# Optimization experiments

Measured on AMD Instinct MI355X. Metric: run time of the kernel, lower is better.

Reference implementation:

```python
import jax, jax.numpy as jnp
import numpy as np
import math

DIM = 384
HEADS = 6
HID = 32  # PositionalEncodingFourier hidden_dim
B, H, W = 16, 56, 56


def _layer_norm(x, g, b, eps=1e-6):
    mu = jnp.mean(x, axis=-1, keepdims=True)
    var = jnp.mean((x - mu) ** 2, axis=-1, keepdims=True)
    return (x - mu) * jax.lax.rsqrt(var + eps) * g + b


def _pos_encoding_fourier(Bb, Hh, Ww, w, b):
    # EdgeNeXt PositionalEncodingFourier with all-False mask: cumsum == arange+1
    scale = 2.0 * math.pi
    y_embed = jnp.arange(1, Hh + 1, dtype=jnp.float32)[:, None] / (Hh + 1e-6) * scale
    x_embed = jnp.arange(1, Ww + 1, dtype=jnp.float32)[None, :] / (Ww + 1e-6) * scale
    dim_t = 10000.0 ** (2.0 * (jnp.arange(HID) // 2).astype(jnp.float32) / HID)
    def enc(e):
        p = jnp.broadcast_to(e, (Hh, Ww))[..., None] / dim_t  # (H,W,HID)
        return jnp.stack([jnp.sin(p[..., 0::2]), jnp.cos(p[..., 1::2])], axis=-1).reshape(Hh, Ww, HID)
    pos = jnp.concatenate([enc(y_embed), enc(x_embed)], axis=-1)  # (H,W,2*HID)
    pos = pos @ w.T + b  # 1x1 conv token_projection as matmul -> (H,W,DIM)
    return jnp.broadcast_to(jnp.transpose(pos, (2, 0, 1))[None], (Bb, DIM, Hh, Ww))


def _forward(x, pos_w, pos_b, ln_g, ln_b, gamma_xca, temperature,
             qkv_w, qkv_b, proj_w, proj_b, rpb_table, conv_w,
             bn_g, bn_b, bn_mean, bn_var, gamma):
    Bb, C, Hh, Ww = x.shape
    N = Hh * Ww
    d = C // HEADS
    xt = jnp.transpose(x.reshape(Bb, C, N), (0, 2, 1))  # (B,N,C)
    pos = _pos_encoding_fourier(Bb, Hh, Ww, pos_w, pos_b)
    xt = xt + jnp.transpose(pos.reshape(Bb, C, N), (0, 2, 1))

    # relative position bias (seq_len T=2): gather (T,T,h) -> expand (h,d^2,T,T)
    # -> nearest interp x0.5 selects element (0,0) -> pixel_shuffle(d) of constant
    # channels == per-head scalar broadcast over the (d,d) channel-attention map.
    T = 2
    rel_idx = jnp.arange(T)[:, None] - jnp.arange(T)[None, :] + T - 1  # (2,2)
    rpb = rpb_table[rel_idx.reshape(-1)].reshape(T, T, HEADS)
    bias = rpb[0, 0][None, :, None, None]  # (1,heads,1,1), broadcasts over (d,d)

    # XCA: cross-covariance (channel) attention
    xn = _layer_norm(xt, ln_g, ln_b)
    qkv = (xn @ qkv_w.T + qkv_b).reshape(Bb, N, 3, HEADS, d)
    qkv = jnp.transpose(qkv, (2, 0, 3, 4, 1))  # (3,B,h,d,N)
    q, k, v = qkv[0], qkv[1], qkv[2]
    q = q / jnp.maximum(jnp.linalg.norm(q, axis=-1, keepdims=True), 1e-12)
    k = k / jnp.maximum(jnp.linalg.norm(k, axis=-1, keepdims=True), 1e-12)
    attn = jnp.einsum('bhdn,bhen->bhde', q, k) * temperature + bias  # (B,h,d,d)
    attn = jax.nn.softmax(attn, axis=-1)
    out = jnp.einsum('bhde,bhen->bhdn', attn, v)  # (B,h,d,N)
    out = jnp.transpose(out, (0, 3, 1, 2)).reshape(Bb, N, C)
    out = out @ proj_w.T + proj_b
    xt = xt + gamma_xca * out

    x2 = jnp.transpose(xt, (0, 2, 1)).reshape(Bb, C, Hh, Ww)
    # pwconv0: conv3x3 (dim->dim, expan_ration hardcoded to 1) + BN(inference) + SiLU
    xi = jax.lax.conv_general_dilated(x2, conv_w, (1, 1), [(1, 1), (1, 1)],
                                      dimension_numbers=('NCHW', 'OIHW', 'NCHW'))
    xi = (xi - bn_mean[None, :, None, None]) * jax.lax.rsqrt(bn_var + 1e-5)[None, :, None, None]
    xi = xi * bn_g[None, :, None, None] + bn_b[None, :, None, None]
    xi = xi * jax.nn.sigmoid(xi)  # SiLU
    x2 = x2 + xi

    # faithful to source: raw reshape (NOT permute) of contiguous NCHW into (B,H,W,C)
    x3 = x2.reshape(Bb, Hh, Ww, C) * gamma
    x3 = jnp.transpose(x3, (0, 3, 1, 2))
    return x + x3


def setup_inputs() -> dict:
    key = jax.random.key(0)
    ks = jax.random.split(key, 10)
    d3 = 3 * DIM
    return {
        'x': jax.random.normal(ks[0], (B, DIM, H, W), jnp.float32),
        'pos_w': jax.random.normal(ks[1], (DIM, 2 * HID), jnp.float32) * 0.05,
        'pos_b': jnp.zeros((DIM,), jnp.float32),
        'ln_g': jnp.ones((DIM,), jnp.float32),
        'ln_b': jnp.zeros((DIM,), jnp.float32),
        'gamma_xca': jax.random.normal(ks[2], (DIM,), jnp.float32) * 0.1,
        'temperature': jnp.ones((HEADS, 1, 1), jnp.float32),
        'qkv_w': jax.random.normal(ks[3], (d3, DIM), jnp.float32) * (DIM ** -0.5),
        'qkv_b': jnp.zeros((d3,), jnp.float32),
        'proj_w': jax.random.normal(ks[4], (DIM, DIM), jnp.float32) * (DIM ** -0.5),
        'proj_b': jnp.zeros((DIM,), jnp.float32),
        'rpb_table': jax.random.normal(ks[5], (3, HEADS), jnp.float32) * 0.02,
        'conv_w': jax.random.normal(ks[6], (DIM, DIM, 3, 3), jnp.float32) * 0.02,
        'bn_g': jnp.ones((DIM,), jnp.float32),
        'bn_b': jnp.zeros((DIM,), jnp.float32),
        'bn_mean': jax.random.normal(ks[7], (DIM,), jnp.float32) * 0.1,
        'bn_var': jax.random.uniform(ks[8], (DIM,), jnp.float32, 0.5, 1.5),
        'gamma': jax.random.normal(ks[9], (DIM,), jnp.float32) * 0.1,
    }


def reference(x, pos_w, pos_b, ln_g, ln_b, gamma_xca, temperature,
              qkv_w, qkv_b, proj_w, proj_b, rpb_table, conv_w,
              bn_g, bn_b, bn_mean, bn_var, gamma):
    return _forward(x, pos_w, pos_b, ln_g, ln_b, gamma_xca, temperature,
                    qkv_w, qkv_b, proj_w, proj_b, rpb_table, conv_w,
                    bn_g, bn_b, bn_mean, bn_var, gamma)
```

## Files before the change

### kernel.cpp

```cpp
#include <hip/hip_runtime.h>
#include <hip/hip_bf16.h>
#include <math.h>

#define DIM 384
#define HEADS 6
#define NN 3136
#define BB 16
#define BH (BB*HEADS)
#define HP 58
#define NP (HP*HP)

typedef __attribute__((ext_vector_type(8))) short short8;
typedef __attribute__((ext_vector_type(4))) short short4v;
typedef __attribute__((ext_vector_type(4))) float f32x4;

__device__ __forceinline__ float bf2f(unsigned short u) {
    union { unsigned int i; float f; } v; v.i = ((unsigned int)u) << 16; return v.f;
}
__device__ __forceinline__ unsigned short f2bf(float f) {
    union { float f; unsigned int i; } v; v.f = f;
    unsigned int r = v.i + 0x7fffu + ((v.i >> 16) & 1u);
    return (unsigned short)(r >> 16);
}
__device__ __forceinline__ void glds16(const unsigned short* g, void* l) {
    __builtin_amdgcn_global_load_lds(
        (const __attribute__((address_space(1))) unsigned int*)g,
        (__attribute__((address_space(3))) unsigned int*)l, 16, 0, 0);
}

__global__ void kw_convert(const float* __restrict__ qkv_w, const float* __restrict__ proj_w,
                           const float* __restrict__ conv_w,
                           unsigned short* __restrict__ Wq, unsigned short* __restrict__ Wp,
                           unsigned short* __restrict__ Wc) {
    int tid = blockIdx.x * 256 + threadIdx.x;
    int stride = gridDim.x * 256;
    for (int i = tid; i < 3*DIM*DIM; i += stride) Wq[i] = f2bf(qkv_w[i]);
    for (int i = tid; i < DIM*DIM; i += stride) Wp[i] = f2bf(proj_w[i]);
    for (int i = tid; i < DIM*DIM*9; i += stride) {
        int ii = i % DIM; int rest = i / DIM; int tap = rest % 9; int o = rest / 9;
        Wc[i] = f2bf(conv_w[(size_t)(o*DIM + ii)*9 + tap]);
    }
}

__global__ void k_pos(const float* __restrict__ pos_w, const float* __restrict__ pos_b,
                      float* __restrict__ P) {
    int n = blockIdx.x; int h = n / 56, w = n % 56;
    __shared__ float feat[64];
    int t = threadIdx.x;
    if (t < 64) {
        int axis = t >> 5;
        int k = t & 31; int i = k >> 1;
        float e = (float)((axis ? w : h) + 1) / 56.000001f * 6.28318530717958647692f;
        float arg = e / powf(10000.0f, (float)i / 16.0f);
        feat[t] = (k & 1) ? cosf(arg) : sinf(arg);
    }
    __syncthreads();
    for (int c = t; c < DIM; c += blockDim.x) {
        float s = pos_b[c];
        #pragma unroll 8
        for (int k = 0; k < 64; k++) s += feat[k] * pos_w[c*64 + k];
        P[(size_t)n*DIM + c] = s;
    }
}

__global__ __launch_bounds__(256) void k_tln(const float* __restrict__ x, const float* __restrict__ P,
                                             const float* __restrict__ g, const float* __restrict__ be,
                                             unsigned short* __restrict__ XTb, unsigned short* __restrict__ XN) {
    __shared__ float tile[32][388];
    int blk = blockIdx.x;
    int b = blk / 98, nt = blk % 98;
    int n0 = nt*32;
    int t = threadIdx.x;
    #pragma unroll
    for (int it = 0; it < 12; it++) {
        int task = it*256 + t;
        int c = task >> 3, seg = task & 7;
        float4 v = *reinterpret_cast<const float4*>(x + ((size_t)(b*DIM + c))*NN + n0 + seg*4);
        tile[seg*4+0][c] = v.x; tile[seg*4+1][c] = v.y;
        tile[seg*4+2][c] = v.z; tile[seg*4+3][c] = v.w;
    }
    __syncthreads();
    int row = t >> 3, sub = t & 7;
    int n = n0 + row;
    f32x4 xp[12];
    float s = 0.f;
    #pragma unroll
    for (int k = 0; k < 12; k++) {
        int c0 = (k*8 + sub)*4;
        float4 tv = *reinterpret_cast<float4*>(&tile[row][c0]);
        float4 pv = *reinterpret_cast<const float4*>(P + (size_t)n*DIM + c0);
        f32x4 xv = {tv.x+pv.x, tv.y+pv.y, tv.z+pv.z, tv.w+pv.w};
        xp[k] = xv;
        s += xv[0]+xv[1]+xv[2]+xv[3];
        unsigned short pkx[4];
        #pragma unroll
        for (int e=0;e<4;e++) pkx[e] = f2bf(xv[e]);
        *reinterpret_cast<short4v*>(XTb + ((size_t)(b*NN + n))*DIM + c0) = *(short4v*)pkx;
    }
    s += __shfl_xor(s, 1, 64); s += __shfl_xor(s, 2, 64); s += __shfl_xor(s, 4, 64);
    float mean = s * (1.0f/384.0f);
    float sq = 0.f;
    #pragma unroll
    for (int k = 0; k < 12; k++) {
        #pragma unroll
        for (int e = 0; e < 4; e++) { float d = xp[k][e]-mean; sq += d*d; }
    }
    sq += __shfl_xor(sq, 1, 64); sq += __shfl_xor(sq, 2, 64); sq += __shfl_xor(sq, 4, 64);
    float rs = rsqrtf(sq * (1.0f/384.0f) + 1e-6f);
    #pragma unroll
    for (int k = 0; k < 12; k++) {
        int c0 = (k*8 + sub)*4;
        unsigned short pk[4];
        #pragma unroll
        for (int e = 0; e < 4; e++)
            pk[e] = f2bf((xp[k][e]-mean)*rs*g[c0+e] + be[c0+e]);
        *reinterpret_cast<short4v*>(XN + ((size_t)(b*NN + n))*DIM + c0) = *(short4v*)pk;
    }
}

template<int MODE>
__global__ __launch_bounds__(256) void k_gemm(
    const unsigned short* __restrict__ A, const unsigned short* __restrict__ Wt,
    const float* __restrict__ bias,
    unsigned short* __restrict__ Qb, unsigned short* __restrict__ Kb, unsigned short* __restrict__ Vt,
    const unsigned short* __restrict__ XTb, const float* __restrict__ gxca, unsigned short* __restrict__ X2p)
{
    __shared__ __align__(16) char smem[35328];
    auto ctA = (float(*)[69])smem;
    auto ctB = (float(*)[130])smem;

    constexpr int NCT = (MODE == 0) ? 9 : 3;
    constexpr int CPX = (MODE == 0) ? 441 : 147;
    int bid = blockIdx.x;
    int orig = (bid & 7)*CPX + (bid >> 3);
    int ct = orig % NCT, mt = orig / NCT;
    int m0 = mt*128, o0 = ct*128;
    int t = threadIdx.x;
    int wave = t >> 6, lane = t & 63;
    int wr = wave >> 1, wc = wave & 1;
    int lr = lane & 15, lg = lane >> 4;

    int r0 = t >> 2;
    int swcol = (((t & 3) ^ ((t >> 3) & 3)) << 3);
    const unsigned short* a0 = A  + (size_t)(m0 + r0)*384 + swcol;
    const unsigned short* a1 = A  + (size_t)(m0 + 64 + r0)*384 + swcol;
    const unsigned short* b0 = Wt + (size_t)(o0 + r0)*384 + swcol;
    const unsigned short* b1 = Wt + (size_t)(o0 + 64 + r0)*384 + swcol;
    int rsw = ((lr >> 1) & 3) << 3;

    auto stage = [&](char* base, int c) {
        glds16(a0 + c, base + wave*1024);
        glds16(a1 + c, base + 4096 + wave*1024);
        glds16(b0 + c, base + 8192 + wave*1024);
        glds16(b1 + c, base + 12288 + wave*1024);
    };

    f32x4 acc[4][4];
    #pragma unroll
    for (int i=0;i<4;i++) for (int j=0;j<4;j++) acc[i][j] = (f32x4){0.f,0.f,0.f,0.f};

    stage(smem, 0);
    __syncthreads();
    for (int kk = 0; kk < 12; kk++) {
        if (kk < 11) stage(smem + ((kk+1)&1)*16384, (kk+1)*32);
        auto As = (unsigned short(*)[32])(smem + (kk&1)*16384);
        auto Bs = (unsigned short(*)[32])(smem + (kk&1)*16384 + 8192);
        short8 af[4], bfv[4];
        #pragma unroll
        for (int i=0;i<4;i++) af[i]  = *(short8*)&As[wr*64 + i*16 + lr][(lg*8) ^ rsw];
        #pragma unroll
        for (int j=0;j<4;j++) bfv[j] = *(short8*)&Bs[wc*64 + j*16 + lr][(lg*8) ^ rsw];
        #pragma unroll
        for (int i=0;i<4;i++)
            #pragma unroll
            for (int j=0;j<4;j++)
                acc[i][j] = __builtin_amdgcn_mfma_f32_16x16x32_bf16(af[i], bfv[j], acc[i][j], 0, 0, 0);
        __syncthreads();
    }

    int comp = (MODE == 0) ? (o0 / DIM) : 0;
    for (int mh = 0; mh < 2; mh++) {
        __syncthreads();
        bool useB = (MODE == 1) || (MODE == 0 && comp == 2);
        if (wr == mh) {
            if (useB) {
                #pragma unroll
                for (int i=0;i<4;i++) for (int j=0;j<4;j++) for (int r=0;r<4;r++)
                    ctB[i*16 + lg*4 + r][wc*64 + j*16 + lr] = acc[i][j][r];
            } else {
                #pragma unroll
                for (int i=0;i<4;i++) for (int j=0;j<4;j++) for (int r=0;r<4;r++)
                    ctA[wc*64 + j*16 + lr][i*16 + lg*4 + r] = acc[i][j][r];
            }
        }
        __syncthreads();
        if (MODE == 1) {
            for (int q = t; q < 1024; q += 256) {
                int row = q >> 4, seg = q & 15;
                int m = m0 + mh*64 + row; int b = m/NN; int n = m - b*NN;
                int py = n/56, px = n - py*56;
                int og0 = o0 + seg*8;
                short8 xvb = *(const short8*)(XTb + (size_t)m*DIM + og0);
                unsigned short pk[8];
                #pragma unroll
                for (int e=0;e<8;e++) {
                    float val = ctB[row][seg*8+e] + bias[og0+e];
                    pk[e] = f2bf(bf2f((unsigned short)xvb[e]) + gxca[og0+e]*val);
                }
                *(short8*)(X2p + ((size_t)(b*NP + (py+1)*HP + px + 1))*DIM + og0) = *(short8*)pk;
            }
        } else if (comp < 2) {
            unsigned short* Dst = (comp == 0) ? Qb : Kb;
            for (int q = t; q < 2048; q += 256) {
                int row = q >> 4, seg = q & 15;
                int og = o0 + row; int rem = og - comp*DIM;
                int hh = rem >> 6, dd = rem & 63;
                int m4 = m0 + mh*64 + seg*4; int b = m4/NN; int n = m4 - b*NN;
                float bv = bias[og];
                unsigned short pk[4];
                #pragma unroll
                for (int e=0;e<4;e++) pk[e] = f2bf(ctA[row][seg*4+e] + bv);
                *(short4v*)(Dst + ((size_t)((b*HEADS + hh)*64 + dd))*NN + n) = *(short4v*)pk;
            }
        } else {
            for (int q = t; q < 1024; q += 256) {
                int row = q >> 4, seg = q & 15;
                int m = m0 + mh*64 + row; int b = m/NN; int n = m - b*NN;
                int og0 = o0 + seg*8; int rem0 = og0 - 2*DIM;
                int hh = rem0 >> 6, dd0 = rem0 & 63;
                unsigned short pk[8];
                #pragma unroll
                for (int e=0;e<8;e++) pk[e] = f2bf(ctB[row][seg*8+e] + bias[og0+e]);
                *(short8*)(Vt + ((size_t)((b*HEADS + hh)*NN + n))*64 + dd0) = *(short8*)pk;
            }
        }
    }
}

__global__ __launch_bounds__(256) void k_pad(unsigned short* __restrict__ X2p) {
    int b = blockIdx.x, part = blockIdx.y;
    unsigned short* base = X2p + (size_t)b*NP*DIM;
    short8 z = {0,0,0,0,0,0,0,0};
    for (int task = part*256 + threadIdx.x; task < 10944; task += 2048) {
        int pos = task / 48, seg = task - pos*48;
        int py, px;
        if (pos < 58)       { py = 0;  px = pos; }
        else if (pos < 116) { py = 57; px = pos - 58; }
        else if (pos < 172) { py = pos - 115; px = 0; }
        else                { py = pos - 171; px = 57; }
        *(short8*)(base + ((size_t)(py*HP + px))*DIM + seg*8) = z;
    }
}

__global__ __launch_bounds__(256, 3) void k_conv(
    const unsigned short* __restrict__ A, const unsigned short* __restrict__ Wt,
    const float* __restrict__ bn_g, const float* __restrict__ bn_b,
    const float* __restrict__ bn_mean, const float* __restrict__ bn_var,
    unsigned short* __restrict__ Yout)
{
    __shared__ __align__(16) char smem[32768];
    auto ctA = (float(*)[69])smem;
    auto X2s = (unsigned short(*)[68])(smem + 17664);

    int bid = blockIdx.x;
    int orig = (bid & 7)*150 + (bid >> 3);
    int ct = orig % 3; int rest = orig / 3;
    int tile = rest % 25; int b = rest / 25;
    int n0 = tile*128, o0 = ct*128;
    int t = threadIdx.x;
    int wave = t >> 6, lane = t & 63;
    int wr = wave >> 1, wc = wave & 1;
    int lr = lane & 15, lg = lane >> 4;
    int qb = n0 + 2*(n0/56);
    const size_t bbase = (size_t)b*NP*DIM;

    int swcol = (((t & 3) ^ ((t >> 3) & 3)) << 3);
    const unsigned short* asrc[4];
    #pragma unroll
    for (int j=0;j<4;j++) {
        int task = j*256 + t;
        int row = task >> 2;
        int q = qb + row; if (q > NP-1) q = NP-1;
        asrc[j] = A + bbase + (size_t)q*DIM + swcol;
    }
    const unsigned short* bsrc0 = Wt + (size_t)(o0 + (t>>2))*3456 + swcol;
    const unsigned short* bsrc1 = Wt + (size_t)(o0 + 64 + (t>>2))*3456 + swcol;

    int qrel[4];
    #pragma unroll
    for (int i=0;i<4;i++) {
        int loc = wr*64 + i*16 + lr;
        int n = n0 + loc; if (n >= NN) n = NN-1;
        qrel[i] = n + 2*(n/56) - qb;
    }

    auto stageA = [&](int c) {
        #pragma unroll
        for (int j=0;j<4;j++) glds16(asrc[j] + c, smem + j*4096 + wave*1024);
    };
    auto stageB = [&](char* base, int off) {
        glds16(bsrc0 + off, base + wave*1024);
        glds16(bsrc1 + off, base + 4096 + wave*1024);
    };

    f32x4 acc[4][4];
    #pragma unroll
    for (int i=0;i<4;i++) for (int j=0;j<4;j++) acc[i][j] = (f32x4){0.f,0.f,0.f,0.f};

    stageA(0); stageB(smem + 16384, 0);
    __syncthreads();
    for (int kk = 0; kk < 12; kk++) {
        int c = kk*32;
        auto Ah = (unsigned short(*)[32])smem;
        #pragma unroll
        for (int tap = 0; tap < 9; tap++) {
            int buf = tap & 1;
            if (tap < 8) stageB(smem + 16384 + (buf^1)*8192, (tap+1)*384 + c);
            auto Bs = (unsigned short(*)[32])(smem + 16384 + buf*8192);
            int toff = (tap/3)*58 + (tap%3);
            short8 af[4], bfv[4];
            #pragma unroll
            for (int j=0;j<4;j++) {
                int brow = wc*64 + j*16 + lr;
                bfv[j] = *(short8*)&Bs[brow][(lg*8) ^ (((brow>>1)&3)<<3)];
            }
            #pragma unroll
            for (int i=0;i<4;i++) {
                int row = qrel[i] + toff;
                af[i] = *(short8*)&Ah[row][(lg*8) ^ (((row>>1)&3)<<3)];
            }
            #pragma unroll
            for (int i=0;i<4;i++)
                #pragma unroll
                for (int j=0;j<4;j++)
                    acc[i][j] = __builtin_amdgcn_mfma_f32_16x16x32_bf16(af[i], bfv[j], acc[i][j], 0, 0, 0);
            __syncthreads();
        }
        if (kk < 11) {
            stageA(c + 32);
            stageB(smem + 16384, c + 32);
            __syncthreads();
        }
    }

    for (int mh = 0; mh < 2; mh++) {
        for (int oh = 0; oh < 2; oh++) {
            __syncthreads();
            if (wr == mh && wc == oh) {
                #pragma unroll
                for (int i=0;i<4;i++) for (int j=0;j<4;j++) for (int r=0;r<4;r++)
                    ctA[j*16 + lr][i*16 + lg*4 + r] = acc[i][j][r];
            }
            for (int q = t; q < 512; q += 256) {
                int row = q >> 3, sg = q & 7;
                int n = n0 + mh*64 + row; int nc = (n < NN) ? n : NN-1;
                int qq = nc + 2*(nc/56) + 59;
                short8 v = *(const short8*)(A + bbase + (size_t)qq*DIM + o0 + oh*64 + sg*8);
                short4v lo = {v[0],v[1],v[2],v[3]}, hi = {v[4],v[5],v[6],v[7]};
                *(short4v*)&X2s[row][sg*8]     = lo;
                *(short4v*)&X2s[row][sg*8 + 4] = hi;
            }
            __syncthreads();
            for (int q = t; q < 512; q += 256) {
                int orow = q >> 3, sg = q & 7;
                int o = o0 + oh*64 + orow;
                int n = n0 + mh*64 + sg*8;
                if (n < NN) {
                    float mean = bn_mean[o], rs = rsqrtf(bn_var[o] + 1e-5f);
                    float gg = bn_g[o], bb2 = bn_b[o];
                    unsigned short pk[8];
                    #pragma unroll
                    for (int e=0;e<8;e++) {
                        float xi = (ctA[orow][sg*8+e] - mean)*rs*gg + bb2;
                        float si = xi / (1.0f + __expf(-xi));
                        pk[e] = f2bf(si + bf2f(X2s[sg*8+e][orow]));
                    }
                    *(short8*)(Yout + ((size_t)(b*DIM + o))*NN + n) = *(short8*)pk;
                }
            }
        }
    }
}

__global__ __launch_bounds__(256) void k_qk(const unsigned short* __restrict__ Qb,
                                            const unsigned short* __restrict__ Kb,
                                            float* __restrict__ Gp, float* __restrict__ Np) {
    int cx = blockIdx.x, bh = blockIdx.y;
    int t = threadIdx.x, wave = t >> 6, lane = t & 63;
    int lr = lane & 15, lg = lane >> 4;
    {
        int row = t >> 1, p = t & 1;
        const unsigned short* src = (row < 64)
            ? Qb + ((size_t)bh*64 + row)*NN + cx*448
            : Kb + ((size_t)bh*64 + (row-64))*NN + cx*448;
        float s = 0.f;
        #pragma unroll
        for (int it = 0; it < 28; it++) {
            short8 v = *(const short8*)(src + p*224 + it*8);
            #pragma unroll
            for (int jj=0;jj<8;jj++) { float f = bf2f((unsigned short)v[jj]); s += f*f; }
        }
        s += __shfl_xor(s, 1, 64);
        if (p == 0) Np[((size_t)bh*7 + cx)*128 + row] = s;
    }
    f32x4 acc[4];
    #pragma unroll
    for (int j=0;j<4;j++) acc[j] = (f32x4){0.f,0.f,0.f,0.f};
    const unsigned short* qrow = Qb + ((size_t)bh*64 + wave*16 + lr)*NN + cx*448;
    const unsigned short* kbase = Kb + (size_t)bh*64*NN + cx*448;
    for (int ks = 0; ks < 14; ks++) {
        short8 a = *(const short8*)(qrow + ks*32 + lg*8);
        #pragma unroll
        for (int j=0;j<4;j++) {
            short8 bfr = *(const short8*)(kbase + (size_t)(j*16+lr)*NN + ks*32 + lg*8);
            acc[j] = __builtin_amdgcn_mfma_f32_16x16x32_bf16(a, bfr, acc[j], 0, 0, 0);
        }
    }
    float* gbase = Gp + ((size_t)bh*7 + cx)*4096;
    #pragma unroll
    for (int j=0;j<4;j++)
        #pragma unroll
        for (int r=0;r<4;r++)
            gbase[(wave*16 + lg*4 + r)*64 + j*16 + lr] = acc[j][r];
}

__global__ __launch_bounds__(256) void k_sm(const float* __restrict__ Gp, const float* __restrict__ Np,
                                            const float* __restrict__ temperature,
                                            const float* __restrict__ rpb,
                                            unsigned short* __restrict__ ATT) {
    int bh = blockIdx.x; int h = bh % HEADS;
    int t = threadIdx.x;
    __shared__ float snorm[128];
    if (t < 128) {
        float s = 0.f;
        #pragma unroll
        for (int cx=0;cx<7;cx++) s += Np[((size_t)bh*7 + cx)*128 + t];
        snorm[t] = fmaxf(sqrtf(s), 1e-12f);
    }
    __syncthreads();
    int dq = t >> 2, de0 = (t & 3) * 16;
    f32x4 g[4];
    #pragma unroll
    for (int i=0;i<4;i++) g[i] = (f32x4){0.f,0.f,0.f,0.f};
    #pragma unroll
    for (int cx=0;cx<7;cx++) {
        const float* base = Gp + ((size_t)bh*7 + cx)*4096 + dq*64 + de0;
        #pragma unroll
        for (int i=0;i<4;i++) {
            float4 v = *(const float4*)(base + i*4);
            g[i][0]+=v.x; g[i][1]+=v.y; g[i][2]+=v.z; g[i][3]+=v.w;
        }
    }
    float temp = temperature[h];
    float bias = rpb[HEADS + h];
    float qn = snorm[dq];
    float lv[16]; float mx = -1e30f;
    #pragma unroll
    for (int i=0;i<4;i++)
        #pragma unroll
        for (int e=0;e<4;e++) {
            int de = de0 + i*4 + e;
            float v = g[i][e] / (qn * snorm[64 + de]) * temp + bias;
            lv[i*4+e] = v; mx = fmaxf(mx, v);
        }
    mx = fmaxf(mx, __shfl_xor(mx, 1, 64));
    mx = fmaxf(mx, __shfl_xor(mx, 2, 64));
    float se = 0.f;
    #pragma unroll
    for (int e=0;e<16;e++) { lv[e] = __expf(lv[e]-mx); se += lv[e]; }
    se += __shfl_xor(se, 1, 64);
    se += __shfl_xor(se, 2, 64);
    float inv = 1.0f/se;
    unsigned short pk[16];
    #pragma unroll
    for (int e=0;e<16;e++) pk[e] = f2bf(lv[e]*inv);
    unsigned short* dst = ATT + ((size_t)bh*64 + dq)*64 + de0;
    *(short8*)dst       = *(short8*)pk;
    *(short8*)(dst + 8) = *(short8*)(pk + 8);
}

__global__ __launch_bounds__(256) void k_pv(const unsigned short* __restrict__ ATT,
                                            const unsigned short* __restrict__ Vt,
                                            unsigned short* __restrict__ XCA) {
    int nt = blockIdx.x, bh = blockIdx.y;
    int b = bh / HEADS, h = bh % HEADS;
    int t = threadIdx.x, wave = t >> 6, lane = t & 63;
    int lr = lane & 15, lg = lane >> 4;
    int n0 = nt*64;
    __shared__ float ctP[64][67];
    f32x4 acc[4];
    for (int i=0;i<4;i++) acc[i] = (f32x4){0.f,0.f,0.f,0.f};
    for (int ks=0; ks<2; ks++) {
        short8 bfr = *reinterpret_cast<const short8*>(Vt + ((size_t)bh*NN + n0 + wave*16 + lr)*64 + ks*32 + lg*8);
        for (int i=0;i<4;i++) {
            short8 a = *reinterpret_cast<const short8*>(ATT + ((size_t)bh*64 + i*16 + lr)*64 + ks*32 + lg*8);
            acc[i] = __builtin_amdgcn_mfma_f32_16x16x32_bf16(a, bfr, acc[i], 0, 0, 0);
        }
    }
    int nl = wave*16 + lr;
    #pragma unroll
    for (int i=0;i<4;i++)
        #pragma unroll
        for (int r=0;r<4;r++) ctP[nl][i*16 + lg*4 + r] = acc[i][r];
    __syncthreads();
    for (int q = t; q < 512; q += 256) {
        int row = q >> 3, seg = q & 7;
        unsigned short pk[8];
        #pragma unroll
        for (int e=0;e<8;e++) pk[e] = f2bf(ctP[row][seg*8+e]);
        *(short8*)(XCA + ((size_t)(b*NN + n0 + row))*DIM + h*64 + seg*8) = *(short8*)pk;
    }
}

__global__ __launch_bounds__(256) void k_final(const float* __restrict__ x, const unsigned short* __restrict__ Yb,
                                               const float* __restrict__ gamma, float* __restrict__ out) {
    int i = blockIdx.x, b = blockIdx.y, kc = blockIdx.z;
    __shared__ float tile[56*193];
    int t = threadIdx.x;
    int k0 = kc*192;
    const unsigned short* ybase = Yb + (size_t)b*DIM*NN + (size_t)i*21504 + k0;
    for (int q = t; q < 56*24; q += 256) {
        int j = q / 24, c8 = (q % 24) * 8;
        short8 v = *(const short8*)(ybase + (size_t)j*384 + c8);
        float* dst = &tile[j*193 + c8];
        #pragma unroll
        for (int e=0;e<8;e++) dst[e] = bf2f((unsigned short)v[e]);
    }
    __syncthreads();
    for (int q = t; q < 192*56; q += 256) {
        int kl = q / 56, j = q % 56;
        int k = k0 + kl;
        size_t gi = ((size_t)(b*DIM + k))*NN + (size_t)i*56 + j;
        out[gi] = x[gi] + gamma[k] * tile[j*193 + kl];
    }
}

extern "C" void kernel_launch(void* const* d_in, const int* in_sizes, int n_in,
                              void* d_out, int out_size, void* d_ws, size_t ws_size,
                              hipStream_t stream) {
    const float* x       = (const float*)d_in[0];
    const float* pos_w   = (const float*)d_in[1];
    const float* pos_b   = (const float*)d_in[2];
    const float* ln_g    = (const float*)d_in[3];
    const float* ln_b    = (const float*)d_in[4];
    const float* gxca    = (const float*)d_in[5];
    const float* temp    = (const float*)d_in[6];
    const float* qkv_w   = (const float*)d_in[7];
    const float* qkv_b   = (const float*)d_in[8];
    const float* proj_w  = (const float*)d_in[9];
    const float* proj_b  = (const float*)d_in[10];
    const float* rpb     = (const float*)d_in[11];
    const float* conv_w  = (const float*)d_in[12];
    const float* bn_g    = (const float*)d_in[13];
    const float* bn_b    = (const float*)d_in[14];
    const float* bn_mean = (const float*)d_in[15];
    const float* bn_var  = (const float*)d_in[16];
    const float* gamma   = (const float*)d_in[17];
    float* out = (float*)d_out;
    char* ws = (char*)d_ws;

    const size_t oP   = 0;
    const size_t oXT  = oP   + 4816896;
    const size_t oXN  = oXT  + 77070336;
    const size_t oQ   = oXN  + 38535168;
    const size_t oK   = oQ   + 38535168;
    const size_t oV   = oK   + 38535168;
    const size_t oATT = oV   + 38535168;
    const size_t oWq  = oATT + 786432;
    const size_t oWp  = oWq  + 884736;
    const size_t oWc  = oWp  + 294912;

    float* P            = (float*)(ws + oP);
    unsigned short* XTb = (unsigned short*)(ws + oXT);
    unsigned short* Yb  = (unsigned short*)(ws + oXT);
    unsigned short* XN  = (unsigned short*)(ws + oXN);
    float* Gp           = (float*)(ws + oXN);
    float* Np           = (float*)(ws + oXN + 11010048);
    unsigned short* XCA = (unsigned short*)(ws + oXN);
    unsigned short* Qb  = (unsigned short*)(ws + oQ);
    unsigned short* X2p = (unsigned short*)(ws + oQ);
    unsigned short* Kb  = (unsigned short*)(ws + oK);
    unsigned short* Vt  = (unsigned short*)(ws + oV);
    unsigned short* ATT = (unsigned short*)(ws + oATT);
    unsigned short* Wq  = (unsigned short*)(ws + oWq);
    unsigned short* Wp  = (unsigned short*)(ws + oWp);
    unsigned short* Wc  = (unsigned short*)(ws + oWc);

    kw_convert<<<256, 256, 0, stream>>>(qkv_w, proj_w, conv_w, Wq, Wp, Wc);
    k_pos<<<NN, 128, 0, stream>>>(pos_w, pos_b, P);
    k_tln<<<BB*98, 256, 0, stream>>>(x, P, ln_g, ln_b, XTb, XN);
    k_gemm<0><<<3528, 256, 0, stream>>>(XN, Wq, qkv_b,
        Qb, Kb, Vt, nullptr, nullptr, nullptr);
    k_qk<<<dim3(7, BH), 256, 0, stream>>>(Qb, Kb, Gp, Np);
    k_sm<<<BH, 256, 0, stream>>>(Gp, Np, temp, rpb, ATT);
    k_pad<<<dim3(BB, 8), 256, 0, stream>>>(X2p);
    k_pv<<<dim3(49, BH), 256, 0, stream>>>(ATT, Vt, XCA);
    k_gemm<1><<<1176, 256, 0, stream>>>(XCA, Wp, proj_b,
        nullptr, nullptr, nullptr, XTb, gxca, X2p);
    k_conv<<<1200, 256, 0, stream>>>(X2p, Wc, bn_g, bn_b, bn_mean, bn_var, Yb);
    k_final<<<dim3(56, BB, 2), 256, 0, stream>>>(x, Yb, gamma, out);
}
```

Measured before the change: 474.1 us.

## Double-buffer conv A tile and use fine-grained vmcnt waits in GEMM loops

In the GEMM kernel, the full __syncthreads is replaced by explicit s_waitcnt vmcnt counts plus raw barriers, so the prefetch of the next stage can stay in flight while the current one is consumed. In the conv kernel, the A tile is now double-buffered: shared memory grows to 48KB, and the next K-slice of A is prefetched at tap 6 instead of after all taps finish. This overlaps global-to-LDS loads with MFMA work. The cost is more LDS per block, which may reduce occupancy under launch_bounds(256,3), and correctness now depends on the hand-counted vmcnt values.

Measured after the change: 459.8 us. 1.03x faster.

```diff
diff --git a/kernel.cpp b/kernel.cpp
--- a/kernel.cpp
+++ b/kernel.cpp
@@ -160,9 +160,15 @@
     for (int i=0;i<4;i++) for (int j=0;j<4;j++) acc[i][j] = (f32x4){0.f,0.f,0.f,0.f};
 
     stage(smem, 0);
-    __syncthreads();
     for (int kk = 0; kk < 12; kk++) {
-        if (kk < 11) stage(smem + ((kk+1)&1)*16384, (kk+1)*32);
+        if (kk < 11) {
+            stage(smem + ((kk+1)&1)*16384, (kk+1)*32);
+            asm volatile("s_waitcnt vmcnt(4)" ::: "memory");
+        } else {
+            asm volatile("s_waitcnt vmcnt(0)" ::: "memory");
+        }
+        __builtin_amdgcn_s_barrier();
+        __builtin_amdgcn_sched_barrier(0);
         auto As = (unsigned short(*)[32])(smem + (kk&1)*16384);
         auto Bs = (unsigned short(*)[32])(smem + (kk&1)*16384 + 8192);
         short8 af[4], bfv[4];
@@ -175,7 +181,8 @@
             #pragma unroll
             for (int j=0;j<4;j++)
                 acc[i][j] = __builtin_amdgcn_mfma_f32_16x16x32_bf16(af[i], bfv[j], acc[i][j], 0, 0, 0);
-        __syncthreads();
+        __builtin_amdgcn_s_barrier();
+        __builtin_amdgcn_sched_barrier(0);
     }
 
     int comp = (MODE == 0) ? (o0 / DIM) : 0;
@@ -258,7 +265,7 @@
     const float* __restrict__ bn_mean, const float* __restrict__ bn_var,
     unsigned short* __restrict__ Yout)
 {
-    __shared__ __align__(16) char smem[32768];
+    __shared__ __align__(16) char smem[49152];
     auto ctA = (float(*)[69])smem;
     auto X2s = (unsigned short(*)[68])(smem + 17664);
 
@@ -294,29 +301,38 @@
         qrel[i] = n + 2*(n/56) - qb;
     }
 
-    auto stageA = [&](int c) {
-        #pragma unroll
-        for (int j=0;j<4;j++) glds16(asrc[j] + c, smem + j*4096 + wave*1024);
+    auto stageA = [&](int bufsel, int c) {
+        #pragma unroll
+        for (int j=0;j<4;j++) glds16(asrc[j] + c, smem + bufsel*16384 + j*4096 + wave*1024);
     };
-    auto stageB = [&](char* base, int off) {
-        glds16(bsrc0 + off, base + wave*1024);
-        glds16(bsrc1 + off, base + 4096 + wave*1024);
+    auto stageB = [&](int slot, int off) {
+        glds16(bsrc0 + off, smem + 32768 + slot*8192 + wave*1024);
+        glds16(bsrc1 + off, smem + 32768 + slot*8192 + 4096 + wave*1024);
     };
 
     f32x4 acc[4][4];
     #pragma unroll
     for (int i=0;i<4;i++) for (int j=0;j<4;j++) acc[i][j] = (f32x4){0.f,0.f,0.f,0.f};
 
-    stageA(0); stageB(smem + 16384, 0);
-    __syncthreads();
+    stageA(0, 0); stageB(0, 0);
     for (int kk = 0; kk < 12; kk++) {
-        int c = kk*32;
-        auto Ah = (unsigned short(*)[32])smem;
+        auto Ah = (unsigned short(*)[32])(smem + (kk&1)*16384);
         #pragma unroll
         for (int tap = 0; tap < 9; tap++) {
-            int buf = tap & 1;
-            if (tap < 8) stageB(smem + 16384 + (buf^1)*8192, (tap+1)*384 + c);
-            auto Bs = (unsigned short(*)[32])(smem + 16384 + buf*8192);
+            if (kk < 11 || tap < 8) {
+                int off = (tap < 8) ? ((tap+1)*384 + kk*32) : ((kk+1)*32);
+                stageB((kk+tap+1)&1, off);
+            }
+            if (tap == 6 && kk < 11) stageA((kk+1)&1, (kk+1)*32);
+            if (kk < 11 && (tap == 6 || tap == 7))
+                asm volatile("s_waitcnt vmcnt(6)" ::: "memory");
+            else if (kk == 11 && tap == 8)
+                asm volatile("s_waitcnt vmcnt(0)" ::: "memory");
+            else
+                asm volatile("s_waitcnt vmcnt(2)" ::: "memory");
+            __builtin_amdgcn_s_barrier();
+            __builtin_amdgcn_sched_barrier(0);
+            auto Bs = (unsigned short(*)[32])(smem + 32768 + ((kk+tap)&1)*8192);
             int toff = (tap/3)*58 + (tap%3);
             short8 af[4], bfv[4];
             #pragma unroll
@@ -334,12 +350,8 @@
                 #pragma unroll
                 for (int j=0;j<4;j++)
                     acc[i][j] = __builtin_amdgcn_mfma_f32_16x16x32_bf16(af[i], bfv[j], acc[i][j], 0, 0, 0);
-            __syncthreads();
-        }
-        if (kk < 11) {
-            stageA(c + 32);
-            stageB(smem + 16384, c + 32);
-            __syncthreads();
+            __builtin_amdgcn_s_barrier();
+            __builtin_amdgcn_sched_barrier(0);
         }
     }
 
```
